# Performance work log

Measured on AMD Instinct MI355X. Metric: run time of the kernel, lower is better.

Reference implementation:

```python
import jax, jax.numpy as jnp
import numpy as np

N_USERS = 100000
N_ITEMS = 50000
N_NODES = N_USERS + N_ITEMS
NNZ = 4000000
BATCH = 16384
DIM = 64
ALPHA = 0.1
K_LAYERS = 3


def setup_inputs() -> dict:
    key = jax.random.key(0)
    ks = jax.random.split(key, 7)
    user_emb = 0.1 * jax.random.normal(ks[0], (N_USERS, DIM), dtype=jnp.float32)
    item_emb = 0.1 * jax.random.normal(ks[1], (N_ITEMS, DIM), dtype=jnp.float32)
    edge_vals = jax.random.uniform(ks[2], (NNZ,), dtype=jnp.float32)
    row = jax.random.randint(ks[3], (NNZ,), 0, N_NODES, dtype=jnp.int32)
    col = jax.random.randint(ks[4], (NNZ,), 0, N_NODES, dtype=jnp.int32)
    users = jax.random.randint(ks[5], (BATCH,), 0, N_USERS, dtype=jnp.int32)
    items = jax.random.randint(ks[6], (BATCH,), 0, N_ITEMS, dtype=jnp.int32)
    return {"user_emb": user_emb, "item_emb": item_emb, "edge_vals": edge_vals,
            "row": row, "col": col, "users": users, "items": items}


def _propagate(user_emb, item_emb, edge_vals, row, col):
    # computer(): concat user/item embeddings, then APPNP/PPR-style propagation
    # x^{k+1} = alpha * x0 + (1-alpha) * A x^k   (A sparse COO, symmetric-normalized)
    x0 = jnp.concatenate([user_emb, item_emb], axis=0)  # [N, d]
    x = x0
    w = edge_vals[:, None]
    for _ in range(K_LAYERS):
        msg = w * x[col]  # gather: [nnz, d]
        agg = jax.ops.segment_sum(msg, row, num_segments=N_NODES)  # scatter-add spmm
        x = ALPHA * x0 + (1.0 - ALPHA) * agg
    return x[:N_USERS], x[N_USERS:]


def reference(user_emb, item_emb, edge_vals, row, col, users, items):
    all_users, all_items = _propagate(user_emb, item_emb, edge_vals, row, col)
    u = all_users[users]   # [B, d]
    i = all_items[items]   # [B, d]
    gamma = jnp.sum(u * i, axis=1)  # [B]
    return gamma
```

## Files before the change

kernel.cpp:

```cpp
#include <hip/hip_runtime.h>

#define N_USERS 100000
#define N_ITEMS 50000
#define N_NODES 150000
#define NNZ_EDGES 4000000
#define BATCH_SZ 16384
#define DIM 64
#define ALPHA 0.1f
#define BETA 0.9f

#define BKT_SHIFT 9
#define BKT_ROWS  (1 << BKT_SHIFT)
#define NBKT      ((N_NODES + BKT_ROWS - 1) >> BKT_SHIFT)
#define BKT_PAD   16
#define BIN_CHUNK 4096
#define N_BIN_BLOCKS ((NNZ_EDGES + BIN_CHUNK - 1) / BIN_CHUNK)

__device__ __forceinline__ unsigned short gtn_f2bf(float f) {
    unsigned int u = __float_as_uint(f);
    u = u + 0x7FFFu + ((u >> 16) & 1u);
    return (unsigned short)(u >> 16);
}

__global__ void gtn_cvt_kernel(const float* __restrict__ xu,
                               const float* __restrict__ xi,
                               unsigned short* __restrict__ x0b) {
    const int total4 = N_NODES * DIM / 4;
    const int boundary4 = N_USERS * DIM / 4;
    for (int i4 = blockIdx.x * blockDim.x + threadIdx.x; i4 < total4;
         i4 += gridDim.x * blockDim.x) {
        const float4 v = (i4 < boundary4)
            ? ((const float4*)xu)[i4]
            : ((const float4*)xi)[i4 - boundary4];
        ushort4 o;
        o.x = gtn_f2bf(v.x);
        o.y = gtn_f2bf(v.y);
        o.z = gtn_f2bf(v.z);
        o.w = gtn_f2bf(v.w);
        ((ushort4*)x0b)[i4] = o;
    }
}

__global__ void gtn_bin_sort_kernel(const int* __restrict__ row,
                                    const int* __restrict__ col,
                                    const float* __restrict__ w,
                                    int2* __restrict__ binned,
                                    int2* __restrict__ blkSeg,
                                    int* __restrict__ bucketTotal) {
    __shared__ int hist[NBKT];
    __shared__ int scanb[512];
    __shared__ int cursor[NBKT];
    __shared__ int2 stage[BIN_CHUNK];
    const int blk = blockIdx.x;
    const int t = threadIdx.x;
    const int chunkStart = blk * BIN_CHUNK;
    const int chunkN = min(BIN_CHUNK, NNZ_EDGES - chunkStart);

    for (int b = t; b < NBKT; b += 512) hist[b] = 0;
    __syncthreads();

    int rloc[BIN_CHUNK / 512];
#pragma unroll
    for (int k = 0; k < BIN_CHUNK / 512; ++k) {
        const int i = t + k * 512;
        int r = -1;
        if (i < chunkN) {
            r = row[chunkStart + i];
            atomicAdd(&hist[r >> BKT_SHIFT], 1);
        }
        rloc[k] = r;
    }
    __syncthreads();

    const int hv = (t < NBKT) ? hist[t] : 0;
    scanb[t] = hv;
    __syncthreads();
    for (int off = 1; off < 512; off <<= 1) {
        const int tv = (t >= off) ? scanb[t - off] : 0;
        __syncthreads();
        scanb[t] += tv;
        __syncthreads();
    }
    if (t < NBKT) {
        const int exc = scanb[t] - hv;
        cursor[t] = exc;
        blkSeg[(size_t)t * N_BIN_BLOCKS + blk] = make_int2(exc, hv);
        if (hv) atomicAdd(&bucketTotal[t * BKT_PAD], hv);
    }
    __syncthreads();

#pragma unroll
    for (int k = 0; k < BIN_CHUNK / 512; ++k) {
        const int i = t + k * 512;
        if (i < chunkN) {
            const int r = rloc[k];
            const int b = r >> BKT_SHIFT;
            const int pos = atomicAdd(&cursor[b], 1);
            stage[pos] = make_int2(col[chunkStart + i] | ((r & (BKT_ROWS - 1)) << 18),
                                   __float_as_int(w[chunkStart + i]));
        }
    }
    __syncthreads();

    int2* dst = binned + (size_t)chunkStart;
#pragma unroll
    for (int k = 0; k < BIN_CHUNK / 512; ++k) {
        const int i = t + k * 512;
        if (i < chunkN) dst[i] = stage[i];
    }
}

__global__ void gtn_bktbase_kernel(const int* __restrict__ bucketTotal,
                                   int* __restrict__ bktBase) {
    __shared__ int s[512];
    const int t = threadIdx.x;
    const int v = (t < NBKT) ? bucketTotal[t * BKT_PAD] : 0;
    s[t] = v;
    __syncthreads();
    for (int off = 1; off < 512; off <<= 1) {
        const int tv = (t >= off) ? s[t - off] : 0;
        __syncthreads();
        s[t] += tv;
        __syncthreads();
    }
    if (t < NBKT) bktBase[t] = s[t] - v;
}

__global__ void gtn_bucket_csr_kernel(const int2* __restrict__ binned,
                                      const int2* __restrict__ blkSeg,
                                      const int* __restrict__ bktBase,
                                      int* __restrict__ rowPtr,
                                      int* __restrict__ cnt,
                                      int2* __restrict__ colw) {
    __shared__ int hist[BKT_ROWS];
    __shared__ int scan[BKT_ROWS];
    __shared__ int cursor[BKT_ROWS];
    const int b = blockIdx.x;
    const int t = threadIdx.x;
    if (t < BKT_ROWS) hist[t] = 0;
    __syncthreads();

    int2 seg = make_int2(0, 0);
    const int2* p0 = binned;
    if (t < N_BIN_BLOCKS) {
        seg = blkSeg[(size_t)b * N_BIN_BLOCKS + t];
        p0 = binned + (size_t)t * BIN_CHUNK + seg.x;
    }
    for (int j = 0; j < seg.y; ++j)
        atomicAdd(&hist[((unsigned)p0[j].x) >> 18], 1);
    __syncthreads();

    const int v = (t < BKT_ROWS) ? hist[t] : 0;
    if (t < BKT_ROWS) scan[t] = v;
    __syncthreads();
    for (int off = 1; off < BKT_ROWS; off <<= 1) {
        int tv = 0;
        if (t < BKT_ROWS && t >= off) tv = scan[t - off];
        __syncthreads();
        if (t < BKT_ROWS) scan[t] += tv;
        __syncthreads();
    }
    if (t < BKT_ROWS) {
        const int g = (b << BKT_SHIFT) + t;
        const int pos0 = bktBase[b] + scan[t] - v;
        if (g < N_NODES) { cnt[g] = v; rowPtr[g] = pos0; }
        cursor[t] = pos0;
    }
    __syncthreads();

    for (int j = 0; j < seg.y; ++j) {
        const int2 ed = p0[j];
        const int inrow = ((unsigned)ed.x) >> 18;
        const int pos = atomicAdd(&cursor[inrow], 1);
        colw[pos] = make_int2(ed.x & 0x3FFFF, ed.y);
    }
}

__device__ __forceinline__ float4 gtn_gather_row_bf16(
        int node, int lane, int sub, int grp,
        const unsigned short* __restrict__ x,
        const int* __restrict__ rowPtr, const int* __restrict__ cnt,
        const int2* __restrict__ colw) {
    const int start = rowPtr[node];
    const int n = cnt[node];
    float4 acc = make_float4(0.f, 0.f, 0.f, 0.f);
    for (int base = 0; base < n; base += 64) {
        const int m = min(64, n - base);
        int2 e = make_int2(0, 0);
        if (lane < m) e = colw[start + base + lane];
        const int nj = (m + 3) >> 2;
        for (int jb = 0; jb < nj; jb += 4) {
            uint2 xv[4];
            float wv[4];
#pragma unroll
            for (int k = 0; k < 4; ++k) {
                const int src = ((jb + k) << 2) + grp;
                const int c = __shfl(e.x, src, 64);
                wv[k] = __int_as_float(__shfl(e.y, src, 64));
                xv[k] = *(const uint2*)(x + ((size_t)c << 6) + (sub << 2));
            }
#pragma unroll
            for (int k = 0; k < 4; ++k) {
                acc.x = fmaf(wv[k], __uint_as_float(xv[k].x << 16), acc.x);
                acc.y = fmaf(wv[k], __uint_as_float(xv[k].x & 0xFFFF0000u), acc.y);
                acc.z = fmaf(wv[k], __uint_as_float(xv[k].y << 16), acc.z);
                acc.w = fmaf(wv[k], __uint_as_float(xv[k].y & 0xFFFF0000u), acc.w);
            }
        }
    }
    return acc;
}

__device__ __forceinline__ float4 gtn_reduce_groups(float4 a) {
    a.x += __shfl_xor(a.x, 16, 64);
    a.y += __shfl_xor(a.y, 16, 64);
    a.z += __shfl_xor(a.z, 16, 64);
    a.w += __shfl_xor(a.w, 16, 64);
    a.x += __shfl_xor(a.x, 32, 64);
    a.y += __shfl_xor(a.y, 32, 64);
    a.z += __shfl_xor(a.z, 32, 64);
    a.w += __shfl_xor(a.w, 32, 64);
    return a;
}

__device__ __forceinline__ void gtn_store_bf16_row(unsigned short* out,
                                                   int node, int sub, float4 o) {
    ushort4 o4;
    o4.x = gtn_f2bf(o.x);
    o4.y = gtn_f2bf(o.y);
    o4.z = gtn_f2bf(o.z);
    o4.w = gtn_f2bf(o.w);
    ((ushort4*)(out + (size_t)node * DIM))[sub] = o4;
}

__global__ void gtn_layer_kernel(const unsigned short* __restrict__ x,
                                 const float* __restrict__ x0u,
                                 const float* __restrict__ x0i,
                                 const int* __restrict__ rowPtr,
                                 const int* __restrict__ cnt,
                                 const int2* __restrict__ colw,
                                 unsigned short* __restrict__ out) {
    const int lane = threadIdx.x & 63;
    const int sub = lane & 15;
    const int grp = lane >> 4;
    const int node = (blockIdx.x * blockDim.x + threadIdx.x) >> 6;
    if (node >= N_NODES) return;
    float4 agg = gtn_gather_row_bf16(node, lane, sub, grp, x, rowPtr, cnt, colw);
    agg = gtn_reduce_groups(agg);
    if (grp == 0) {
        const float4 x0v = (node < N_USERS)
            ? ((const float4*)(x0u + (size_t)node * DIM))[sub]
            : ((const float4*)(x0i + (size_t)(node - N_USERS) * DIM))[sub];
        float4 o;
        o.x = ALPHA * x0v.x + BETA * agg.x;
        o.y = ALPHA * x0v.y + BETA * agg.y;
        o.z = ALPHA * x0v.z + BETA * agg.z;
        o.w = ALPHA * x0v.w + BETA * agg.w;
        gtn_store_bf16_row(out, node, sub, o);
    }
}

__global__ void gtn_l3_dot_kernel(const unsigned short* __restrict__ x,
                                  const float* __restrict__ x0u,
                                  const float* __restrict__ x0i,
                                  const int* __restrict__ rowPtr,
                                  const int* __restrict__ cnt,
                                  const int2* __restrict__ colw,
                                  const int* __restrict__ users,
                                  const int* __restrict__ items,
                                  float* __restrict__ out) {
    const int lane = threadIdx.x & 63;
    const int sub = lane & 15;
    const int grp = lane >> 4;
    const int b = (blockIdx.x * blockDim.x + threadIdx.x) >> 6;
    if (b >= BATCH_SZ) return;
    const int u = users[b];
    const int it = items[b] + N_USERS;

    float4 au = gtn_gather_row_bf16(u, lane, sub, grp, x, rowPtr, cnt, colw);
    au = gtn_reduce_groups(au);
    float4 ai = gtn_gather_row_bf16(it, lane, sub, grp, x, rowPtr, cnt, colw);
    ai = gtn_reduce_groups(ai);

    const float4 x0uv = ((const float4*)(x0u + (size_t)u * DIM))[sub];
    const float4 x0iv = ((const float4*)(x0i + (size_t)(it - N_USERS) * DIM))[sub];
    float4 vu, vi;
    vu.x = ALPHA * x0uv.x + BETA * au.x;  vi.x = ALPHA * x0iv.x + BETA * ai.x;
    vu.y = ALPHA * x0uv.y + BETA * au.y;  vi.y = ALPHA * x0iv.y + BETA * ai.y;
    vu.z = ALPHA * x0uv.z + BETA * au.z;  vi.z = ALPHA * x0iv.z + BETA * ai.z;
    vu.w = ALPHA * x0uv.w + BETA * au.w;  vi.w = ALPHA * x0iv.w + BETA * ai.w;

    float p = vu.x * vi.x + vu.y * vi.y + vu.z * vi.z + vu.w * vi.w;
    p += __shfl_xor(p, 1, 64);
    p += __shfl_xor(p, 2, 64);
    p += __shfl_xor(p, 4, 64);
    p += __shfl_xor(p, 8, 64);
    if (lane == 0) out[b] = p;
}

extern "C" void kernel_launch(void* const* d_in, const int* in_sizes, int n_in,
                              void* d_out, int out_size, void* d_ws, size_t ws_size,
                              hipStream_t stream) {
    const float* user_emb  = (const float*)d_in[0];
    const float* item_emb  = (const float*)d_in[1];
    const float* edge_vals = (const float*)d_in[2];
    const int*   row       = (const int*)d_in[3];
    const int*   col       = (const int*)d_in[4];
    const int*   users     = (const int*)d_in[5];
    const int*   items     = (const int*)d_in[6];
    float* out = (float*)d_out;

    char* p = (char*)d_ws;
    unsigned short* x0b  = (unsigned short*)p; p += (size_t)N_NODES * DIM * 2;
    unsigned short* bufA = (unsigned short*)p; p += (size_t)N_NODES * DIM * 2;
    unsigned short* bufB = (unsigned short*)p; p += (size_t)N_NODES * DIM * 2;
    int2*  colw        = (int2*)p; p += (size_t)NNZ_EDGES * sizeof(int2);
    int2*  binned      = (int2*)p; p += (size_t)NNZ_EDGES * sizeof(int2);
    int2*  blkSeg      = (int2*)p; p += (size_t)NBKT * N_BIN_BLOCKS * sizeof(int2);
    int*   bucketTotal = (int*)p;  p += (size_t)NBKT * BKT_PAD * sizeof(int);
    int*   bktBase     = (int*)p;  p += 512 * sizeof(int);
    int*   cnt         = (int*)p;  p += (size_t)N_NODES * sizeof(int);
    int*   rowPtr      = (int*)p;  p += (size_t)N_NODES * sizeof(int);

    const dim3 blk(256);

    hipMemsetAsync(bucketTotal, 0, (size_t)NBKT * BKT_PAD * sizeof(int), stream);
    gtn_bin_sort_kernel<<<dim3(N_BIN_BLOCKS), dim3(512), 0, stream>>>(
        row, col, edge_vals, binned, blkSeg, bucketTotal);
    gtn_cvt_kernel<<<dim3(2048), blk, 0, stream>>>(user_emb, item_emb, x0b);
    gtn_bktbase_kernel<<<dim3(1), dim3(512), 0, stream>>>(bucketTotal, bktBase);
    gtn_bucket_csr_kernel<<<dim3(NBKT), dim3(1024), 0, stream>>>(
        binned, blkSeg, bktBase, rowPtr, cnt, colw);

    const dim3 layerGrid((N_NODES * 64 + 255) / 256);
    gtn_layer_kernel<<<layerGrid, blk, 0, stream>>>(
        x0b, user_emb, item_emb, rowPtr, cnt, colw, bufA);
    gtn_layer_kernel<<<layerGrid, blk, 0, stream>>>(
        bufA, user_emb, item_emb, rowPtr, cnt, colw, bufB);
    const dim3 dotGrid((BATCH_SZ * 64) / 256);
    gtn_l3_dot_kernel<<<dotGrid, blk, 0, stream>>>(
        bufB, user_emb, item_emb, rowPtr, cnt, colw, users, items, out);
}
```

Measured before the change: 328.6 us.

## Flatten bucket edges across threads with scan and binary search in CSR build

The bucket-to-CSR kernel used to give each thread one bin-block segment and walk it serially, which left work uneven across threads and made memory access poorly coalesced. Now the segment lengths are prefix-scanned in shared memory, and each of 1024 threads takes edges strided across the flattened range, finding its segment by binary search. Edges are kept in registers between the histogram pass and the scatter pass, so they are read from global memory only once. Buckets grow to 1024 rows, which means fewer and larger blocks. The register array sets a hard cap of 30720 edges per bucket and raises register pressure.

Result: faster. 278.7 us (-15.2%).

```diff
diff --git a/kernel.cpp b/kernel.cpp
--- a/kernel.cpp
+++ b/kernel.cpp
@@ -9,12 +9,14 @@
 #define ALPHA 0.1f
 #define BETA 0.9f
 
-#define BKT_SHIFT 9
+#define BKT_SHIFT 10
 #define BKT_ROWS  (1 << BKT_SHIFT)
 #define NBKT      ((N_NODES + BKT_ROWS - 1) >> BKT_SHIFT)
 #define BKT_PAD   16
 #define BIN_CHUNK 4096
 #define N_BIN_BLOCKS ((NNZ_EDGES + BIN_CHUNK - 1) / BIN_CHUNK)
+#define SEG_MAX   1024
+#define EDGES_PER_THREAD 30
 
 __device__ __forceinline__ unsigned short gtn_f2bf(float f) {
     unsigned int u = __float_as_uint(f);
@@ -132,47 +134,69 @@
                                       int* __restrict__ rowPtr,
                                       int* __restrict__ cnt,
                                       int2* __restrict__ colw) {
+    __shared__ int incl[SEG_MAX];
+    __shared__ int segIdx[SEG_MAX];
     __shared__ int hist[BKT_ROWS];
     __shared__ int scan[BKT_ROWS];
     __shared__ int cursor[BKT_ROWS];
     const int b = blockIdx.x;
     const int t = threadIdx.x;
-    if (t < BKT_ROWS) hist[t] = 0;
-    __syncthreads();
 
     int2 seg = make_int2(0, 0);
-    const int2* p0 = binned;
-    if (t < N_BIN_BLOCKS) {
-        seg = blkSeg[(size_t)b * N_BIN_BLOCKS + t];
-        p0 = binned + (size_t)t * BIN_CHUNK + seg.x;
-    }
-    for (int j = 0; j < seg.y; ++j)
-        atomicAdd(&hist[((unsigned)p0[j].x) >> 18], 1);
-    __syncthreads();
-
-    const int v = (t < BKT_ROWS) ? hist[t] : 0;
-    if (t < BKT_ROWS) scan[t] = v;
+    if (t < N_BIN_BLOCKS) seg = blkSeg[(size_t)b * N_BIN_BLOCKS + t];
+    segIdx[t] = t * BIN_CHUNK + seg.x;
+    incl[t] = seg.y;
+    hist[t] = 0;
+    __syncthreads();
+    for (int off = 1; off < SEG_MAX; off <<= 1) {
+        const int tv = (t >= off) ? incl[t - off] : 0;
+        __syncthreads();
+        incl[t] += tv;
+        __syncthreads();
+    }
+    const int n = incl[SEG_MAX - 1];
+
+    int2 e[EDGES_PER_THREAD];
+#pragma unroll
+    for (int k = 0; k < EDGES_PER_THREAD; ++k) {
+        const int i = t + k * 1024;
+        if (i < n) {
+            int s = 0;
+#pragma unroll
+            for (int st = 512; st > 0; st >>= 1) {
+                const int c = s + st;
+                if (c <= SEG_MAX && incl[c - 1] <= i) s = c;
+            }
+            const int base = s ? incl[s - 1] : 0;
+            e[k] = binned[(size_t)segIdx[s] + (i - base)];
+            atomicAdd(&hist[((unsigned)e[k].x) >> 18], 1);
+        }
+    }
+    __syncthreads();
+
+    const int v = hist[t];
+    scan[t] = v;
     __syncthreads();
     for (int off = 1; off < BKT_ROWS; off <<= 1) {
-        int tv = 0;
-        if (t < BKT_ROWS && t >= off) tv = scan[t - off];
-        __syncthreads();
-        if (t < BKT_ROWS) scan[t] += tv;
-        __syncthreads();
-    }
-    if (t < BKT_ROWS) {
-        const int g = (b << BKT_SHIFT) + t;
-        const int pos0 = bktBase[b] + scan[t] - v;
-        if (g < N_NODES) { cnt[g] = v; rowPtr[g] = pos0; }
-        cursor[t] = pos0;
-    }
-    __syncthreads();
-
-    for (int j = 0; j < seg.y; ++j) {
-        const int2 ed = p0[j];
-        const int inrow = ((unsigned)ed.x) >> 18;
-        const int pos = atomicAdd(&cursor[inrow], 1);
-        colw[pos] = make_int2(ed.x & 0x3FFFF, ed.y);
+        const int tv = (t >= off) ? scan[t - off] : 0;
+        __syncthreads();
+        scan[t] += tv;
+        __syncthreads();
+    }
+    const int g = (b << BKT_SHIFT) + t;
+    const int pos0 = bktBase[b] + scan[t] - v;
+    if (g < N_NODES) { cnt[g] = v; rowPtr[g] = pos0; }
+    cursor[t] = pos0;
+    __syncthreads();
+
+#pragma unroll
+    for (int k = 0; k < EDGES_PER_THREAD; ++k) {
+        const int i = t + k * 1024;
+        if (i < n) {
+            const int inrow = ((unsigned)e[k].x) >> 18;
+            const int pos = atomicAdd(&cursor[inrow], 1);
+            colw[pos] = make_int2(e[k].x & 0x3FFFF, e[k].y);
+        }
     }
 }
 
```
